# Kernel optimization log

Hardware: AMD Instinct MI355X
Metric: run time of the kernel (lower is better)

The kernel has to match this reference:

```python
import jax, jax.numpy as jnp
import numpy as np


def setup_inputs() -> dict:
    key = jax.random.key(0)
    # flow field [B, 2, H, W]; randn gives sub-pixel to few-pixel displacements
    input1 = jax.random.normal(key, (8, 2, 1080, 1920), dtype=jnp.float32)
    return {"input1": input1}


def reference(input1):
    # DAIN-style flow projection (forward warping / splatting).
    # For each source pixel (x, y) with flow (u, v), the target location is
    # (x+u, y+v). The NEGATED flow is scattered into the 4 integer neighbors
    # (floor/ceil in each axis) of the target, with a count accumulator; the
    # result is averaged by count. fillhole=0 (requires_grad=True path).
    B, C, H, W = input1.shape  # C == 2
    dtype = input1.dtype

    fx = jnp.arange(W, dtype=dtype)[None, None, :] + input1[:, 0]  # [B,H,W]
    fy = jnp.arange(H, dtype=dtype)[None, :, None] + input1[:, 1]  # [B,H,W]
    xf = jnp.floor(fx).astype(jnp.int32)
    yf = jnp.floor(fy).astype(jnp.int32)

    boff = (jnp.arange(B, dtype=jnp.int32) * (H * W))[:, None, None]  # batch offset
    neg_u = (-input1[:, 0]).reshape(-1)
    neg_v = (-input1[:, 1]).reshape(-1)

    acc_u = jnp.zeros((B * H * W,), dtype=dtype)
    acc_v = jnp.zeros((B * H * W,), dtype=dtype)
    cnt = jnp.zeros((B * H * W,), dtype=dtype)

    for dx in (0, 1):
        for dy in (0, 1):
            tx = xf + dx
            ty = yf + dy
            valid = (tx >= 0) & (tx < W) & (ty >= 0) & (ty < H)
            idx = jnp.where(valid, boff + ty * W + tx, 0).reshape(-1)
            w = valid.astype(dtype).reshape(-1)
            acc_u = acc_u.at[idx].add(neg_u * w)
            acc_v = acc_v.at[idx].add(neg_v * w)
            cnt = cnt.at[idx].add(w)

    count = cnt.reshape(B, 1, H, W)
    out = jnp.stack([acc_u.reshape(B, H, W), acc_v.reshape(B, H, W)], axis=1)
    out = jnp.where(count > 0, out / jnp.where(count > 0, count, 1.0), 0.0)
    return out
```

## Files before the change

### kernel.cpp

```cpp
#include <hip/hip_runtime.h>

#define B_DIM 8
#define H_DIM 1080
#define W_DIM 1920
#define HW (H_DIM * W_DIM)

#define TW 128
#define TH 16
#define R  8
#define SW (TW + 2 * R)
#define SH (TH + 2 * R)
#define THRESH 7.0f
#define OVF_CAP 1024

#define FRAC_BITS 11
#define FIELD_BIAS (1 << 18)

struct OvfRec { int b; int p; };

__global__ void __launch_bounds__(256, 8)
flowproj_gather(const float* __restrict__ in, float* __restrict__ out,
                unsigned* __restrict__ ovf_cnt, OvfRec* __restrict__ recs) {
    __shared__ unsigned long long s_acc[TH * TW];

    const int tid = threadIdx.x;
    const int x0 = blockIdx.x * TW;
    const int y0 = blockIdx.y * TH;
    const int b  = blockIdx.z;

    #pragma unroll
    for (int i = tid; i < TW * TH; i += 256) s_acc[i] = 0ull;
    __syncthreads();

    const float* up = in + (size_t)b * 2 * HW;
    const float* vp = up + HW;

    #pragma unroll 2
    for (int i = tid; i < SW * SH; i += 256) {
        int sx = x0 - R + (i % SW);
        int sy = y0 - R + (i / SW);
        if (sx < 0 || sx >= W_DIM || sy < 0 || sy >= H_DIM) continue;
        int p = sy * W_DIM + sx;
        float u = up[p];
        float v = vp[p];
        if (fabsf(u) > THRESH || fabsf(v) > THRESH) {
            if (sx >= x0 && sx < x0 + TW && sy >= y0 && sy < y0 + TH) {
                unsigned slot = atomicAdd(ovf_cnt, 1u);
                if (slot < OVF_CAP) { recs[slot].b = b; recs[slot].p = p; }
            }
            continue;
        }
        int xf = (int)floorf((float)sx + u);
        int yf = (int)floorf((float)sy + v);

        int iu = __float2int_rn(-u * (float)(1 << FRAC_BITS));
        int iv = __float2int_rn(-v * (float)(1 << FRAC_BITS));
        unsigned long long enc =
            (1ull << 48) |
            ((unsigned long long)(unsigned)(iv + FIELD_BIAS) << 24) |
            (unsigned long long)(unsigned)(iu + FIELD_BIAS);

        int bx = xf - x0;
        int by = yf - y0;
        #pragma unroll
        for (int dy = 0; dy < 2; ++dy) {
            int ty = by + dy;
            if ((unsigned)ty >= TH) continue;
            #pragma unroll
            for (int dx = 0; dx < 2; ++dx) {
                int tx = bx + dx;
                if ((unsigned)tx >= TW) continue;
                atomicAdd(&s_acc[ty * TW + tx], enc);
            }
        }
    }
    __syncthreads();

    float* ou = out + (size_t)b * 2 * HW;
    float* ov = ou + HW;
    const float inv_scale = 1.0f / (float)(1 << FRAC_BITS);
    #pragma unroll
    for (int i = tid; i < TW * TH; i += 256) {
        int lx = i % TW;
        int ly = i / TW;
        int ox = x0 + lx;
        int oy = y0 + ly;
        if (ox >= W_DIM || oy >= H_DIM) continue;
        unsigned long long s = s_acc[i];
        int cnt  = (int)(s >> 48);
        int vraw = (int)((s >> 24) & 0xFFFFFF);
        int uraw = (int)(s & 0xFFFFFF);
        int o = oy * W_DIM + ox;
        if (cnt > 0) {
            float inv = 1.0f / (float)cnt;
            float usum = (float)(uraw - (cnt << 18)) * inv_scale;
            float vsum = (float)(vraw - (cnt << 18)) * inv_scale;
            ou[o] = usum * inv;
            ov[o] = vsum * inv;
        } else {
            ou[o] = 0.0f;
            ov[o] = 0.0f;
        }
    }
}

__device__ inline int rec_cells(const float* in, int b, int p, int* cg) {
    const float* up = in + (size_t)b * 2 * HW;
    int sx = p % W_DIM, sy = p / W_DIM;
    float u = up[p], v = up[HW + p];
    int xf = (int)floorf((float)sx + u);
    int yf = (int)floorf((float)sy + v);
    int n = 0;
    for (int dy = 0; dy < 2; ++dy)
        for (int dx = 0; dx < 2; ++dx) {
            int tx = xf + dx, ty = yf + dy;
            if (tx >= 0 && tx < W_DIM && ty >= 0 && ty < H_DIM)
                cg[n++] = ty * W_DIM + tx;
        }
    return n;
}

__global__ void flowproj_fixup(const float* __restrict__ in, float* __restrict__ out,
                               const unsigned* __restrict__ ovf_cnt,
                               const OvfRec* __restrict__ recs) {
    if (threadIdx.x != 0 || blockIdx.x != 0) return;
    int n = (int)min(*ovf_cnt, (unsigned)OVF_CAP);
    for (int r = 0; r < n; ++r) {
        int b = recs[r].b, p = recs[r].p;
        int cg[4];
        int nc = rec_cells(in, b, p, cg);
        for (int ci = 0; ci < nc; ++ci) {
            int g = cg[ci];
            bool seen = false;
            for (int r2 = 0; r2 <= r && !seen; ++r2) {
                if (recs[r2].b != b) continue;
                int cg2[4];
                int nc2 = rec_cells(in, b, recs[r2].p, cg2);
                int lim = (r2 == r) ? ci : nc2;
                for (int j = 0; j < lim; ++j)
                    if (cg2[j] == g) { seen = true; break; }
            }
            if (seen) continue;
            float du = 0.0f, dv = 0.0f, dc = 0.0f;
            const float* up = in + (size_t)b * 2 * HW;
            for (int r2 = r; r2 < n; ++r2) {
                if (recs[r2].b != b) continue;
                int cg2[4];
                int nc2 = rec_cells(in, b, recs[r2].p, cg2);
                for (int j = 0; j < nc2; ++j)
                    if (cg2[j] == g) {
                        du -= up[recs[r2].p];
                        dv -= up[HW + recs[r2].p];
                        dc += 1.0f;
                        break;
                    }
            }
            int ty = g / W_DIM, tx = g % W_DIM;
            float c = 0.0f;
            for (int qy = max(0, ty - R); qy <= min(H_DIM - 1, ty + R); ++qy)
                for (int qx = max(0, tx - R); qx <= min(W_DIM - 1, tx + R); ++qx) {
                    int q = qy * W_DIM + qx;
                    float qu = up[q], qv = up[HW + q];
                    if (fabsf(qu) > THRESH || fabsf(qv) > THRESH) continue;
                    int qxf = (int)floorf((float)qx + qu);
                    int qyf = (int)floorf((float)qy + qv);
                    if ((tx == qxf || tx == qxf + 1) && (ty == qyf || ty == qyf + 1))
                        c += 1.0f;
                }
            float* ou = out + (size_t)b * 2 * HW;
            float* ov = ou + HW;
            float au = (c > 0.0f) ? ou[g] * c : 0.0f;
            float av = (c > 0.0f) ? ov[g] * c : 0.0f;
            float ncnt = c + dc;
            ou[g] = (au + du) / ncnt;
            ov[g] = (av + dv) / ncnt;
        }
    }
}

extern "C" void kernel_launch(void* const* d_in, const int* in_sizes, int n_in,
                              void* d_out, int out_size, void* d_ws, size_t ws_size,
                              hipStream_t stream) {
    const float* in = (const float*)d_in[0];
    float* out = (float*)d_out;
    unsigned* ovf = (unsigned*)d_ws;
    OvfRec* recs = (OvfRec*)((char*)d_ws + 16);

    hipMemsetAsync(d_ws, 0, 16, stream);

    dim3 grid(W_DIM / TW, (H_DIM + TH - 1) / TH, B_DIM);
    flowproj_gather<<<grid, 256, 0, stream>>>(in, out, ovf, recs);
    flowproj_fixup<<<1, 64, 0, stream>>>(in, out, ovf, recs);
}
```

Before: 261.6 us.

## Use per-block overflow records with a parallel fixup and 64x32 tiles

The tile shape changes from 128x16 to 64x32, which cuts the halo overhead per output. The global atomic overflow counter becomes a per-block shared counter with per-block record slots, and that removes the memset and the global atomic contention. The single-thread serial fixup becomes a per-slot parallel fixup that recomputes each affected cell directly. Risks: each fixup thread scans every block's counter (about 8K entries) for every cell, more than 8 overflow records per block are silently dropped, the narrower bias field could overflow, and duplicate cells written by different threads produce benign races.

```diff
diff --git a/kernel.cpp b/kernel.cpp
--- a/kernel.cpp
+++ b/kernel.cpp
@@ -5,48 +5,53 @@
 #define W_DIM 1920
 #define HW (H_DIM * W_DIM)
 
-#define TW 128
-#define TH 16
+#define TW 64
+#define TH 32
 #define R  8
 #define SW (TW + 2 * R)
 #define SH (TH + 2 * R)
 #define THRESH 7.0f
-#define OVF_CAP 1024
+#define GX (W_DIM / TW)
+#define GY ((H_DIM + TH - 1) / TH)
+#define NBLK (GX * GY * B_DIM)
+#define RECS_PER_BLK 8
 
 #define FRAC_BITS 11
-#define FIELD_BIAS (1 << 18)
-
-struct OvfRec { int b; int p; };
+#define FIELD_BIAS (1 << 15)
 
 __global__ void __launch_bounds__(256, 8)
 flowproj_gather(const float* __restrict__ in, float* __restrict__ out,
-                unsigned* __restrict__ ovf_cnt, OvfRec* __restrict__ recs) {
+                int* __restrict__ cnt_arr, int2* __restrict__ recs) {
     __shared__ unsigned long long s_acc[TH * TW];
+    __shared__ int s_ovf;
 
     const int tid = threadIdx.x;
     const int x0 = blockIdx.x * TW;
     const int y0 = blockIdx.y * TH;
     const int b  = blockIdx.z;
+    const int blin = (b * GY + blockIdx.y) * GX + blockIdx.x;
 
     #pragma unroll
     for (int i = tid; i < TW * TH; i += 256) s_acc[i] = 0ull;
+    if (tid == 0) s_ovf = 0;
     __syncthreads();
 
     const float* up = in + (size_t)b * 2 * HW;
     const float* vp = up + HW;
 
-    #pragma unroll 2
     for (int i = tid; i < SW * SH; i += 256) {
         int sx = x0 - R + (i % SW);
         int sy = y0 - R + (i / SW);
-        if (sx < 0 || sx >= W_DIM || sy < 0 || sy >= H_DIM) continue;
+        if ((unsigned)sx >= (unsigned)W_DIM || (unsigned)sy >= (unsigned)H_DIM)
+            continue;
         int p = sy * W_DIM + sx;
         float u = up[p];
         float v = vp[p];
         if (fabsf(u) > THRESH || fabsf(v) > THRESH) {
             if (sx >= x0 && sx < x0 + TW && sy >= y0 && sy < y0 + TH) {
-                unsigned slot = atomicAdd(ovf_cnt, 1u);
-                if (slot < OVF_CAP) { recs[slot].b = b; recs[slot].p = p; }
+                int slot = atomicAdd(&s_ovf, 1);
+                if (slot < RECS_PER_BLK)
+                    recs[blin * RECS_PER_BLK + slot] = make_int2(b, p);
             }
             continue;
         }
@@ -70,22 +75,24 @@
             for (int dx = 0; dx < 2; ++dx) {
                 int tx = bx + dx;
                 if ((unsigned)tx >= TW) continue;
-                atomicAdd(&s_acc[ty * TW + tx], enc);
+                atomicAdd(&s_acc[(ty << 6) + tx], enc);
             }
         }
     }
     __syncthreads();
+
+    if (tid == 0) cnt_arr[blin] = s_ovf;
 
     float* ou = out + (size_t)b * 2 * HW;
     float* ov = ou + HW;
     const float inv_scale = 1.0f / (float)(1 << FRAC_BITS);
     #pragma unroll
     for (int i = tid; i < TW * TH; i += 256) {
-        int lx = i % TW;
-        int ly = i / TW;
+        int lx = i & (TW - 1);
+        int ly = i >> 6;
+        int oy = y0 + ly;
+        if (oy >= H_DIM) continue;
         int ox = x0 + lx;
-        int oy = y0 + ly;
-        if (ox >= W_DIM || oy >= H_DIM) continue;
         unsigned long long s = s_acc[i];
         int cnt  = (int)(s >> 48);
         int vraw = (int)((s >> 24) & 0xFFFFFF);
@@ -93,8 +100,8 @@
         int o = oy * W_DIM + ox;
         if (cnt > 0) {
             float inv = 1.0f / (float)cnt;
-            float usum = (float)(uraw - (cnt << 18)) * inv_scale;
-            float vsum = (float)(vraw - (cnt << 18)) * inv_scale;
+            float usum = (float)(uraw - (cnt << 15)) * inv_scale;
+            float vsum = (float)(vraw - (cnt << 15)) * inv_scale;
             ou[o] = usum * inv;
             ov[o] = vsum * inv;
         } else {
@@ -104,77 +111,64 @@
     }
 }
 
-__device__ inline int rec_cells(const float* in, int b, int p, int* cg) {
-    const float* up = in + (size_t)b * 2 * HW;
-    int sx = p % W_DIM, sy = p / W_DIM;
-    float u = up[p], v = up[HW + p];
-    int xf = (int)floorf((float)sx + u);
-    int yf = (int)floorf((float)sy + v);
-    int n = 0;
-    for (int dy = 0; dy < 2; ++dy)
-        for (int dx = 0; dx < 2; ++dx) {
-            int tx = xf + dx, ty = yf + dy;
-            if (tx >= 0 && tx < W_DIM && ty >= 0 && ty < H_DIM)
-                cg[n++] = ty * W_DIM + tx;
-        }
-    return n;
-}
+__global__ void __launch_bounds__(256)
+flowproj_fixup(const float* __restrict__ in, float* __restrict__ out,
+               const int* __restrict__ cnt_arr, const int2* __restrict__ recs) {
+    int slot = blockIdx.x * 256 + threadIdx.x;
+    if (slot >= NBLK) return;
+    int c = cnt_arr[slot];
+    if (c <= 0) return;
+    c = min(c, RECS_PER_BLK);
 
-__global__ void flowproj_fixup(const float* __restrict__ in, float* __restrict__ out,
-                               const unsigned* __restrict__ ovf_cnt,
-                               const OvfRec* __restrict__ recs) {
-    if (threadIdx.x != 0 || blockIdx.x != 0) return;
-    int n = (int)min(*ovf_cnt, (unsigned)OVF_CAP);
-    for (int r = 0; r < n; ++r) {
-        int b = recs[r].b, p = recs[r].p;
-        int cg[4];
-        int nc = rec_cells(in, b, p, cg);
-        for (int ci = 0; ci < nc; ++ci) {
-            int g = cg[ci];
-            bool seen = false;
-            for (int r2 = 0; r2 <= r && !seen; ++r2) {
-                if (recs[r2].b != b) continue;
-                int cg2[4];
-                int nc2 = rec_cells(in, b, recs[r2].p, cg2);
-                int lim = (r2 == r) ? ci : nc2;
-                for (int j = 0; j < lim; ++j)
-                    if (cg2[j] == g) { seen = true; break; }
+    for (int r = 0; r < c; ++r) {
+        int2 rec = recs[slot * RECS_PER_BLK + r];
+        int b = rec.x, p = rec.y;
+        const float* up = in + (size_t)b * 2 * HW;
+        const float* vp = up + HW;
+        int sx = p % W_DIM, sy = p / W_DIM;
+        float u = up[p], v = vp[p];
+        int xf = (int)floorf((float)sx + u);
+        int yf = (int)floorf((float)sy + v);
+
+        for (int dy = 0; dy < 2; ++dy)
+            for (int dx = 0; dx < 2; ++dx) {
+                int tx = xf + dx, ty = yf + dy;
+                if (tx < 0 || tx >= W_DIM || ty < 0 || ty >= H_DIM) continue;
+                float su = 0.0f, sv = 0.0f, cn = 0.0f;
+                for (int qy = max(0, ty - R); qy <= min(H_DIM - 1, ty + R); ++qy)
+                    for (int qx = max(0, tx - R); qx <= min(W_DIM - 1, tx + R); ++qx) {
+                        int q = qy * W_DIM + qx;
+                        float qu = up[q], qv = vp[q];
+                        if (fabsf(qu) > THRESH || fabsf(qv) > THRESH) continue;
+                        int qxf = (int)floorf((float)qx + qu);
+                        int qyf = (int)floorf((float)qy + qv);
+                        if ((tx == qxf || tx == qxf + 1) && (ty == qyf || ty == qyf + 1)) {
+                            su -= qu; sv -= qv; cn += 1.0f;
+                        }
+                    }
+                for (int s2 = 0; s2 < NBLK; ++s2) {
+                    int c2 = cnt_arr[s2];
+                    if (c2 <= 0) continue;
+                    c2 = min(c2, RECS_PER_BLK);
+                    for (int r2 = 0; r2 < c2; ++r2) {
+                        int2 rec2 = recs[s2 * RECS_PER_BLK + r2];
+                        if (rec2.x != b) continue;
+                        int p2 = rec2.y;
+                        int sx2 = p2 % W_DIM, sy2 = p2 / W_DIM;
+                        float u2 = up[p2], v2 = vp[p2];
+                        int xf2 = (int)floorf((float)sx2 + u2);
+                        int yf2 = (int)floorf((float)sy2 + v2);
+                        if ((tx == xf2 || tx == xf2 + 1) && (ty == yf2 || ty == yf2 + 1)) {
+                            su -= u2; sv -= v2; cn += 1.0f;
+                        }
+                    }
+                }
+                float* ou = out + (size_t)b * 2 * HW;
+                float* ov = ou + HW;
+                int g = ty * W_DIM + tx;
+                if (cn > 0.0f) { ou[g] = su / cn; ov[g] = sv / cn; }
+                else           { ou[g] = 0.0f;   ov[g] = 0.0f; }
             }
-            if (seen) continue;
-            float du = 0.0f, dv = 0.0f, dc = 0.0f;
-            const float* up = in + (size_t)b * 2 * HW;
-            for (int r2 = r; r2 < n; ++r2) {
-                if (recs[r2].b != b) continue;
-                int cg2[4];
-                int nc2 = rec_cells(in, b, recs[r2].p, cg2);
-                for (int j = 0; j < nc2; ++j)
-                    if (cg2[j] == g) {
-                        du -= up[recs[r2].p];
-                        dv -= up[HW + recs[r2].p];
-                        dc += 1.0f;
-                        break;
-                    }
-            }
-            int ty = g / W_DIM, tx = g % W_DIM;
-            float c = 0.0f;
-            for (int qy = max(0, ty - R); qy <= min(H_DIM - 1, ty + R); ++qy)
-                for (int qx = max(0, tx - R); qx <= min(W_DIM - 1, tx + R); ++qx) {
-                    int q = qy * W_DIM + qx;
-                    float qu = up[q], qv = up[HW + q];
-                    if (fabsf(qu) > THRESH || fabsf(qv) > THRESH) continue;
-                    int qxf = (int)floorf((float)qx + qu);
-                    int qyf = (int)floorf((float)qy + qv);
-                    if ((tx == qxf || tx == qxf + 1) && (ty == qyf || ty == qyf + 1))
-                        c += 1.0f;
-                }
-            float* ou = out + (size_t)b * 2 * HW;
-            float* ov = ou + HW;
-            float au = (c > 0.0f) ? ou[g] * c : 0.0f;
-            float av = (c > 0.0f) ? ov[g] * c : 0.0f;
-            float ncnt = c + dc;
-            ou[g] = (au + du) / ncnt;
-            ov[g] = (av + dv) / ncnt;
-        }
     }
 }
 
@@ -183,12 +177,10 @@
                               hipStream_t stream) {
     const float* in = (const float*)d_in[0];
     float* out = (float*)d_out;
-    unsigned* ovf = (unsigned*)d_ws;
-    OvfRec* recs = (OvfRec*)((char*)d_ws + 16);
+    int* cnt_arr = (int*)d_ws;
+    int2* recs = (int2*)((char*)d_ws + 32768);
 
-    hipMemsetAsync(d_ws, 0, 16, stream);
-
-    dim3 grid(W_DIM / TW, (H_DIM + TH - 1) / TH, B_DIM);
-    flowproj_gather<<<grid, 256, 0, stream>>>(in, out, ovf, recs);
-    flowproj_fixup<<<1, 64, 0, stream>>>(in, out, ovf, recs);
+    dim3 grid(GX, GY, B_DIM);
+    flowproj_gather<<<grid, 256, 0, stream>>>(in, out, cnt_arr, recs);
+    flowproj_fixup<<<(NBLK + 255) / 256, 256, 0, stream>>>(in, out, cnt_arr, recs);
 }
```

New measurement: 252.0 us. -3.7%, faster.
